# Kernel tuning notes

Measured on AMD Instinct MI355X. Metric: run time of the kernel, lower is better.

## Reference

```python
import jax, jax.numpy as jnp
import numpy as np

N = 10000
E = 320000
D = 256   # hidden_dim
H = 4     # heads
C = D // H
NL = 3    # gat layers
EPS = 1e-5


def _ln(x, g, b):
    m = x.mean(-1, keepdims=True)
    v = ((x - m) ** 2).mean(-1, keepdims=True)
    return (x - m) / jnp.sqrt(v + EPS) * g + b


def setup_inputs() -> dict:
    key = jax.random.key(0)
    ks = iter(jax.random.split(key, 64))
    rn = lambda shape, s=0.05: jax.random.normal(next(ks), shape, dtype=jnp.float32) * s
    inp = dict(
        x=jax.random.normal(next(ks), (N, 10), dtype=jnp.float32),
        edge_index=jax.random.randint(next(ks), (2, E), 0, N),
        edge_attr=jax.random.uniform(next(ks), (E, 3), dtype=jnp.float32),
        agent_features=jax.random.normal(next(ks), (1, 10), dtype=jnp.float32),
        # node encoder
        enc_w=rn((10, D)), enc_b=jnp.zeros(D), enc_g=jnp.ones(D), enc_bt=jnp.zeros(D),
        # adaptive virtual node
        vn_base=jnp.zeros(D), vn_w1=rn((D, D)), vn_b1=jnp.zeros(D),
        vn_g=jnp.ones(D), vn_bt=jnp.zeros(D), vn_w2=rn((D, D)), vn_b2=jnp.zeros(D),
        # stacked GAT layer params
        gat_w=rn((NL, D, D)), att_src=rn((NL, H, C)), att_dst=rn((NL, H, C)),
        att_edge=rn((NL, H, C)), edge_w=rn((NL, 3, D)), gat_b=jnp.zeros((NL, D)),
        ln_g=jnp.ones((NL, D)), ln_b=jnp.zeros((NL, D)),
        # agent encoder
        ag_w=rn((10, D)), ag_b=jnp.zeros(D), ag_g=jnp.ones(D), ag_bt=jnp.zeros(D),
        # dueling heads (jk_dim = D*(NL+1) + D)
        v_w1=rn((D * (NL + 2), D)), v_b1=jnp.zeros(D), v_g=jnp.ones(D), v_bt=jnp.zeros(D),
        v_w2=rn((D, 1)), v_b2=jnp.zeros(1),
        a_w1=rn((D * (NL + 2), D)), a_b1=jnp.zeros(D), a_g=jnp.ones(D), a_bt=jnp.zeros(D),
        a_w2=rn((D, 9)), a_b2=jnp.zeros(9),
    )
    return inp


def _gat_layer(h, src, dst, eattr, lin_w, a_s, a_d, a_e, e_w, bias, n_seg):
    xs = (h @ lin_w).reshape(-1, H, C)                       # [Nt,H,C]
    al_s = (xs * a_s).sum(-1)                                # [Nt,H]
    al_d = (xs * a_d).sum(-1)
    ee = (eattr @ e_w).reshape(-1, H, C)                     # [Et,H,C]
    al_e = (ee * a_e).sum(-1)                                # [Et,H]
    alpha = jax.nn.leaky_relu(al_s[src] + al_d[dst] + al_e, 0.2)
    mx = jax.ops.segment_max(alpha, dst, num_segments=n_seg)
    a = jnp.exp(alpha - mx[dst])
    s = jax.ops.segment_sum(a, dst, num_segments=n_seg)
    a = a / (s[dst] + 1e-16)
    msg = xs[src] * a[:, :, None]                            # [Et,H,C]
    out = jax.ops.segment_sum(msg, dst, num_segments=n_seg)
    return out.reshape(n_seg, D) + bias


def reference(x, edge_index, edge_attr, agent_features,
              enc_w, enc_b, enc_g, enc_bt,
              vn_base, vn_w1, vn_b1, vn_g, vn_bt, vn_w2, vn_b2,
              gat_w, att_src, att_dst, att_edge, edge_w, gat_b, ln_g, ln_b,
              ag_w, ag_b, ag_g, ag_bt,
              v_w1, v_b1, v_g, v_bt, v_w2, v_b2,
              a_w1, a_b1, a_g, a_bt, a_w2, a_b2):
    n = x.shape[0]
    nt = n + 1  # + virtual node
    h0 = jax.nn.relu(_ln(x @ enc_w + enc_b, enc_g, enc_bt))
    ctx = h0.mean(0)
    ad = jnp.tanh(jax.nn.relu(_ln(ctx @ vn_w1 + vn_b1, vn_g, vn_bt)) @ vn_w2 + vn_b2)
    vn = vn_base + ad
    h = jnp.concatenate([h0, vn[None]], axis=0)              # [Nt,D]

    # virtual-node edges (bidirectional) with edge_attr = [0.5,0,0]
    ar = jnp.arange(n)
    vfull = jnp.full((n,), n, dtype=edge_index.dtype)
    src0 = jnp.concatenate([edge_index[0], vfull, ar])
    dst0 = jnp.concatenate([edge_index[1], ar, vfull])
    veattr = jnp.concatenate([jnp.full((2 * n, 1), 0.5), jnp.zeros((2 * n, 2))], axis=1)
    eattr0 = jnp.concatenate([edge_attr, veattr], axis=0)

    # GATConv add_self_loops with fill_value='mean' (mean of incoming edge_attr)
    deg = jax.ops.segment_sum(jnp.ones_like(dst0, dtype=jnp.float32), dst0, num_segments=nt)
    loop_attr = jax.ops.segment_sum(eattr0, dst0, num_segments=nt) / jnp.maximum(deg, 1.0)[:, None]
    loops = jnp.arange(nt, dtype=edge_index.dtype)
    src = jnp.concatenate([src0, loops])
    dst = jnp.concatenate([dst0, loops])
    eattr = jnp.concatenate([eattr0, loop_attr], axis=0)

    outs = [h]
    for i in range(NL):
        hn = _gat_layer(h, src, dst, eattr, gat_w[i], att_src[i], att_dst[i],
                        att_edge[i], edge_w[i], gat_b[i], nt)
        hn = _ln(hn, ln_g[i], ln_b[i])
        h = jax.nn.relu(hn + h)
        outs.append(h)
    jk = jnp.concatenate(outs, axis=-1)                      # [Nt, D*(NL+1)]

    global_repr = jk[-1][None]                               # virtual node row
    agent = jax.nn.relu(_ln(agent_features @ ag_w + ag_b, ag_g, ag_bt))
    comb = jnp.concatenate([global_repr, agent], axis=-1)
    val = jax.nn.relu(_ln(comb @ v_w1 + v_b1, v_g, v_bt)) @ v_w2 + v_b2
    adv = jax.nn.relu(_ln(comb @ a_w1 + a_b1, a_g, a_bt)) @ a_w2 + a_b2
    return val + (adv - adv.mean(axis=1, keepdims=True))
```

## Files before the change

kernel.cpp:

```cpp
#include <hip/hip_runtime.h>
#include <math.h>

#define NN 10000
#define EE 320000
#define DD 256
#define NT 10001
#define E1C (EE + NN)
#define E2C (EE + 2 * NN)
#define ETC (E2C + NT)
#define VB 157
#define RB 2500

typedef __attribute__((ext_vector_type(8))) short s16x8;
typedef __attribute__((ext_vector_type(4))) float f32x4;

__device__ __forceinline__ unsigned short f2bf(float f) {
    unsigned u = __float_as_uint(f);
    return (unsigned short)((u + 0x7FFFu + ((u >> 16) & 1u)) >> 16);
}
__device__ __forceinline__ float bf2f(unsigned short u) {
    return __uint_as_float((unsigned)u << 16);
}

__device__ __forceinline__ float wave_sum(float v) {
#pragma unroll
    for (int o = 32; o > 0; o >>= 1) v += __shfl_down(v, o, 64);
    return v;
}
__device__ __forceinline__ float blk_sum256(float v, float* sm4) {
    v = wave_sum(v);
    int lane = threadIdx.x & 63, w = threadIdx.x >> 6;
    __syncthreads();
    if (lane == 0) sm4[w] = v;
    __syncthreads();
    return sm4[0] + sm4[1] + sm4[2] + sm4[3];
}
__device__ __forceinline__ float2 blk_sum2(float a, float b, float2* sm4) {
#pragma unroll
    for (int o = 32; o > 0; o >>= 1) {
        a += __shfl_down(a, o, 64);
        b += __shfl_down(b, o, 64);
    }
    int lane = threadIdx.x & 63, w = threadIdx.x >> 6;
    __syncthreads();
    if (lane == 0) sm4[w] = make_float2(a, b);
    __syncthreads();
    float2 r;
    r.x = sm4[0].x + sm4[1].x + sm4[2].x + sm4[3].x;
    r.y = sm4[0].y + sm4[1].y + sm4[2].y + sm4[3].y;
    return r;
}

__global__ void __launch_bounds__(256) k_enc(
        const float* __restrict__ x, const float* __restrict__ wenc,
        const float* __restrict__ bia, const float* __restrict__ g,
        const float* __restrict__ bt, float* __restrict__ h,
        unsigned short* __restrict__ hb) {
    int t = threadIdx.x, lane = t & 63, wv = t >> 6;
    int v = blockIdx.x * 4 + wv;
    if (v >= NN) return;
    float xv = (lane < 10) ? x[v * 10 + lane] : 0.f;
    float4 acc = *(const float4*)(bia + lane * 4);
#pragma unroll
    for (int k = 0; k < 10; k++) {
        float xk = __shfl(xv, k, 64);
        float4 wk = *(const float4*)(wenc + k * DD + lane * 4);
        acc.x += xk * wk.x; acc.y += xk * wk.y; acc.z += xk * wk.z; acc.w += xk * wk.w;
    }
    float s1 = acc.x + acc.y + acc.z + acc.w;
    float s2 = acc.x * acc.x + acc.y * acc.y + acc.z * acc.z + acc.w * acc.w;
#pragma unroll
    for (int o = 32; o > 0; o >>= 1) {
        s1 += __shfl_xor(s1, o, 64);
        s2 += __shfl_xor(s2, o, 64);
    }
    float m = s1 * (1.f / DD);
    float var = s2 * (1.f / DD) - m * m;
    float rs = rsqrtf(var + 1e-5f);
    float4 g4 = *(const float4*)(g + lane * 4);
    float4 b4 = *(const float4*)(bt + lane * 4);
    float4 r4;
    r4.x = fmaxf((acc.x - m) * rs * g4.x + b4.x, 0.f);
    r4.y = fmaxf((acc.y - m) * rs * g4.y + b4.y, 0.f);
    r4.z = fmaxf((acc.z - m) * rs * g4.z + b4.z, 0.f);
    r4.w = fmaxf((acc.w - m) * rs * g4.w + b4.w, 0.f);
    *(float4*)(h + (size_t)v * DD + lane * 4) = r4;
    ushort4 u4;
    u4.x = f2bf(r4.x); u4.y = f2bf(r4.y); u4.z = f2bf(r4.z); u4.w = f2bf(r4.w);
    *(ushort4*)(hb + (size_t)v * DD + lane * 4) = u4;
}

__global__ void __launch_bounds__(256) k_ctx1deg(const float* __restrict__ h,
                                                 float* __restrict__ part,
                                                 const int* __restrict__ ei,
                                                 int* __restrict__ degi) {
    __shared__ float4 sm[4][64];
    int t = threadIdx.x, lane = t & 63, w = t >> 6;
    int b = blockIdx.x;
    float4 acc = make_float4(0.f, 0.f, 0.f, 0.f);
    for (int v = b * 4 + w; v < NN; v += 1024) {
        float4 hv = *(const float4*)(h + (size_t)v * DD + lane * 4);
        acc.x += hv.x; acc.y += hv.y; acc.z += hv.z; acc.w += hv.w;
    }
    sm[w][lane] = acc;
    __syncthreads();
    if (t < 64) {
        float4 a0 = sm[0][t], a1 = sm[1][t], a2 = sm[2][t], a3 = sm[3][t];
        float4 r;
        r.x = a0.x + a1.x + a2.x + a3.x;
        r.y = a0.y + a1.y + a2.y + a3.y;
        r.z = a0.z + a1.z + a2.z + a3.z;
        r.w = a0.w + a1.w + a2.w + a3.w;
        *(float4*)(part + (size_t)b * DD + t * 4) = r;
    }
    for (int e = b * 256 + t; e < EE; e += 256 * 256)
        atomicAdd(&degi[ei[EE + e]], 1);
}

__global__ void k_vn(const float* __restrict__ part,
                     const float* __restrict__ w1, const float* __restrict__ b1,
                     const float* __restrict__ g, const float* __restrict__ bt,
                     const float* __restrict__ w2, const float* __restrict__ b2,
                     const float* __restrict__ vnb,
                     float* __restrict__ h, unsigned short* __restrict__ hb,
                     float* __restrict__ comb) {
    __shared__ float2 sm4[4];
    __shared__ float cs[DD];
    __shared__ float t[DD];
    int j = threadIdx.x;
    float c = 0.f;
    for (int b = 0; b < 256; b++) c += part[(size_t)b * DD + j];
    cs[j] = c * (1.f / NN);
    __syncthreads();
    float acc = b1[j];
    for (int k = 0; k < DD; k++) acc += cs[k] * w1[k * DD + j];
    float2 mm = blk_sum2(acc, acc * acc, sm4);
    float m = mm.x * (1.f / DD);
    float var = mm.y * (1.f / DD) - m * m;
    float y = fmaxf((acc - m) * rsqrtf(var + 1e-5f) * g[j] + bt[j], 0.f);
    t[j] = y;
    __syncthreads();
    float a2 = b2[j];
    for (int k = 0; k < DD; k++) a2 += t[k] * w2[k * DD + j];
    float vn = vnb[j] + tanhf(a2);
    h[(size_t)NN * DD + j] = vn;
    hb[(size_t)NN * DD + j] = f2bf(vn);
    comb[j] = vn;
}

__global__ void k_scan(const int* __restrict__ degi, int* __restrict__ offs,
                       int* __restrict__ cursor) {
    __shared__ int wsum[16];
    __shared__ int running_s;
    int t = threadIdx.x, lane = t & 63, w = t >> 6;
    if (t == 0) running_s = 0;
    __syncthreads();
    for (int base = 0; base < NT; base += 1024) {
        int v = base + t;
        int val = 0;
        if (v < NN) val = degi[v] + 2;
        else if (v == NN) val = NN + 1;
        int x = val;
#pragma unroll
        for (int o = 1; o < 64; o <<= 1) {
            int y = __shfl_up(x, o, 64);
            if (lane >= o) x += y;
        }
        if (lane == 63) wsum[w] = x;
        __syncthreads();
        int prefix = running_s;
        for (int ww = 0; ww < w; ww++) prefix += wsum[ww];
        if (v <= NN) { int e0 = prefix + x - val; offs[v] = e0; cursor[v] = e0; }
        __syncthreads();
        if (t == 0) {
            int s = 0;
            for (int i = 0; i < 16; i++) s += wsum[i];
            running_s += s;
        }
        __syncthreads();
    }
    if (threadIdx.x == 0) offs[NT] = running_s;
}

__global__ void k_scatter(const int* __restrict__ ei, int* __restrict__ cursor,
                          int* __restrict__ ssrc, int* __restrict__ seid) {
    int e = blockIdx.x * 256 + threadIdx.x;
    if (e >= EE) return;
    int src = ei[e], dst = ei[EE + e];
    int pos = atomicAdd(&cursor[dst], 1);
    ssrc[pos] = src;
    seid[pos] = e;
}

__global__ void k_flattr(const int* __restrict__ offs, int* __restrict__ ssrc,
                         int* __restrict__ seid,
                         const float* __restrict__ ea, float* __restrict__ lattr) {
    int t = threadIdx.x, lane = t & 63, w = t >> 6;
    int v = blockIdx.x * 4 + w;
    if (v > NN) return;
    int bN = offs[NN];
    if (v == NN) {
        if (lane == 0) {
            lattr[v * 3] = 0.5f; lattr[v * 3 + 1] = 0.f; lattr[v * 3 + 2] = 0.f;
            ssrc[bN + NN] = NN; seid[bN + NN] = E2C + NN;
        }
        return;
    }
    int b0 = offs[v], e1 = offs[v + 1];
    if (lane == 0) {
        ssrc[e1 - 2] = NN; seid[e1 - 2] = EE + v;
        ssrc[e1 - 1] = v;  seid[e1 - 1] = E2C + v;
        ssrc[bN + v] = v;  seid[bN + v] = E1C + v;
    }
    int cnt = e1 - b0 - 2;
    float s0 = 0.f, s1 = 0.f, s2 = 0.f;
    for (int i = lane; i < cnt; i += 64) {
        int e = seid[b0 + i];
        s0 += ea[e * 3];
        s1 += ea[e * 3 + 1];
        s2 += ea[e * 3 + 2];
    }
    s0 = wave_sum(s0); s1 = wave_sum(s1); s2 = wave_sum(s2);
    if (lane == 0) {
        float inv = 1.f / (float)(cnt + 1);
        lattr[v * 3]     = (s0 + 0.5f) * inv;
        lattr[v * 3 + 1] = s1 * inv;
        lattr[v * 3 + 2] = s2 * inv;
    }
}

__global__ void k_wconv(const float* __restrict__ gw, unsigned short* __restrict__ wt,
                        const float* __restrict__ ew, const float* __restrict__ ae,
                        float* __restrict__ wd) {
    int b = blockIdx.x, j = threadIdx.x;
    if (b == 768) {
        if (j >= 36) return;
        int l = j / 12, k = (j / 4) % 3, h = j % 4;
        float s = 0.f;
        for (int c = 0; c < 64; c++)
            s += ew[l * 768 + k * DD + h * 64 + c] * ae[l * DD + h * 64 + c];
        wd[j] = s;
        return;
    }
    int l = b >> 8, k = b & 255;
    float v = gw[l * 65536 + k * 256 + j];
    wt[l * 65536 + j * 256 + k] = f2bf(v);
}

__global__ void k_edot(const int* __restrict__ seid, const float* __restrict__ ea,
                       const float* __restrict__ lattr, const float* __restrict__ wd,
                       unsigned short* __restrict__ edot) {
    int p = blockIdx.x * 256 + threadIdx.x;
    if (p >= ETC) return;
    int e = seid[p];
    float a0, a1, a2;
    if (e < EE)       { a0 = ea[e * 3]; a1 = ea[e * 3 + 1]; a2 = ea[e * 3 + 2]; }
    else if (e < E2C) { a0 = 0.5f; a1 = 0.f; a2 = 0.f; }
    else              { int v = e - E2C; a0 = lattr[v * 3]; a1 = lattr[v * 3 + 1]; a2 = lattr[v * 3 + 2]; }
#pragma unroll
    for (int l = 0; l < 3; l++) {
        ushort4 o;
        o.x = f2bf(a0 * wd[l * 12 + 0] + a1 * wd[l * 12 + 4] + a2 * wd[l * 12 + 8]);
        o.y = f2bf(a0 * wd[l * 12 + 1] + a1 * wd[l * 12 + 5] + a2 * wd[l * 12 + 9]);
        o.z = f2bf(a0 * wd[l * 12 + 2] + a1 * wd[l * 12 + 6] + a2 * wd[l * 12 + 10]);
        o.w = f2bf(a0 * wd[l * 12 + 3] + a1 * wd[l * 12 + 7] + a2 * wd[l * 12 + 11]);
        *(ushort4*)(edot + (size_t)l * ETC * 4 + (size_t)p * 4) = o;
    }
}

__global__ void __launch_bounds__(256) k_gemm_mfma(
        const unsigned short* __restrict__ hb, const unsigned short* __restrict__ wt,
        const float* __restrict__ as_, const float* __restrict__ ad_,
        unsigned short* __restrict__ xsb, float* __restrict__ als, float* __restrict__ ald) {
    __shared__ unsigned short tile[64][128];
    int bx = blockIdx.x;
    int v0 = (bx >> 1) * 64;
    int n0 = (bx & 1) * 128;
    int t = threadIdx.x, lane = t & 63, w = t >> 6;
    int rbase = v0 + w * 16;
    int li = lane & 15, g = lane >> 4;
    int arow = rbase + li; if (arow > NN) arow = NN;
    int koff = g * 8;
    const unsigned short* aptr = hb + (size_t)arow * DD + koff;
    const unsigned short* bptr = wt + (size_t)(n0 + li) * DD + koff;
    f32x4 acc[8];
#pragma unroll
    for (int n = 0; n < 8; n++) acc[n] = (f32x4){0.f, 0.f, 0.f, 0.f};
#pragma unroll
    for (int kb = 0; kb < 8; kb++) {
        s16x8 af = *(const s16x8*)(aptr + kb * 32);
#pragma unroll
        for (int n = 0; n < 8; n++) {
            s16x8 bf = *(const s16x8*)(bptr + (size_t)n * 16 * DD + kb * 32);
            acc[n] = __builtin_amdgcn_mfma_f32_16x16x32_bf16(af, bf, acc[n], 0, 0, 0);
        }
    }
    float asv[8], adv[8];
#pragma unroll
    for (int n = 0; n < 8; n++) { asv[n] = as_[n0 + n * 16 + li]; adv[n] = ad_[n0 + n * 16 + li]; }
    int hg0 = n0 >> 6;
#pragma unroll
    for (int r = 0; r < 4; r++) {
        int vrow = rbase + 4 * g + r;
#pragma unroll
        for (int h = 0; h < 2; h++) {
            float ps = acc[4 * h][r] * asv[4 * h] + acc[4 * h + 1][r] * asv[4 * h + 1]
                     + acc[4 * h + 2][r] * asv[4 * h + 2] + acc[4 * h + 3][r] * asv[4 * h + 3];
            float pd = acc[4 * h][r] * adv[4 * h] + acc[4 * h + 1][r] * adv[4 * h + 1]
                     + acc[4 * h + 2][r] * adv[4 * h + 2] + acc[4 * h + 3][r] * adv[4 * h + 3];
#pragma unroll
            for (int o = 1; o < 16; o <<= 1) {
                ps += __shfl_xor(ps, o, 64);
                pd += __shfl_xor(pd, o, 64);
            }
            if (li == 0 && vrow <= NN) { als[vrow * 4 + hg0 + h] = ps; ald[vrow * 4 + hg0 + h] = pd; }
        }
    }
#pragma unroll
    for (int n = 0; n < 8; n++)
#pragma unroll
        for (int r = 0; r < 4; r++)
            tile[w * 16 + 4 * g + r][n * 16 + li] = f2bf(acc[n][r]);
#pragma unroll
    for (int it = 0; it < 4; it++) {
        int flat = it * 64 + lane;
        int row = w * 16 + (flat >> 4);
        int c8 = flat & 15;
        int vrow = v0 + row;
        if (vrow <= NN)
            *(uint4*)(xsb + (size_t)vrow * DD + n0 + c8 * 8) = *(const uint4*)(&tile[row][c8 * 8]);
    }
}

__global__ void __launch_bounds__(256) k_msg(
        const int* __restrict__ offs, const int* __restrict__ ssrc,
        const unsigned short* __restrict__ edotL,
        const float* __restrict__ als, const float* __restrict__ ald,
        const unsigned short* __restrict__ xsb,
        const float* __restrict__ bias, const float* __restrict__ g,
        const float* __restrict__ bt, const float* __restrict__ hin,
        float* __restrict__ hout, unsigned short* __restrict__ hbout,
        float* __restrict__ pvacc, float* __restrict__ pws) {
    int b = blockIdx.x;
    int t = threadIdx.x, lane = t & 63, w = t >> 6;
    if (b >= RB) {
        int sub = lane >> 5, l32 = lane & 31, slot = w * 2 + sub;
        int hh = l32 >> 3;
        __shared__ float red[4][8][33];
        __shared__ float wsred[4][4];
        int bb = b - RB;
        int b0 = offs[NN];
        float adh = ald[NN * 4 + hh];
        int i0 = bb * 64, i1 = i0 + 64;
        if (i1 > NN + 1) i1 = NN + 1;
        float acc[8];
#pragma unroll
        for (int q = 0; q < 8; q++) acc[q] = 0.f;
        float swt = 0.f;
        for (int i = i0 + slot; i < i1; i += 8) {
            float a = als[i * 4 + hh] + bf2f(edotL[(size_t)(b0 + i) * 4 + hh]) + adh;
            a = a > 0.f ? a : 0.2f * a;
            float wt = __expf(a);
            uint4 xq = *(const uint4*)(xsb + (size_t)i * DD + l32 * 8);
            const unsigned short* xp = (const unsigned short*)&xq;
#pragma unroll
            for (int q = 0; q < 8; q++) acc[q] += wt * bf2f(xp[q]);
            if ((l32 & 7) == 0) swt += wt;
        }
#pragma unroll
        for (int q = 0; q < 8; q++) acc[q] += __shfl_xor(acc[q], 32, 64);
        swt += __shfl_xor(swt, 32, 64);
        if (sub == 0) {
#pragma unroll
            for (int q = 0; q < 8; q++) red[w][q][l32] = acc[q];
            if ((l32 & 7) == 0) wsred[w][hh] = swt;
        }
        __syncthreads();
        int c = t, q = c & 7, l = c >> 3;
        pvacc[(size_t)bb * DD + c] = red[0][q][l] + red[1][q][l] + red[2][q][l] + red[3][q][l];
        if (t < 4) pws[bb * 4 + t] = wsred[0][t] + wsred[1][t] + wsred[2][t] + wsred[3][t];
        return;
    }
    __shared__ int   lsrc[4][64];
    __shared__ float lw[4][64][4];
    int v = b * 4 + w;
    int b0 = offs[v], deg = offs[v + 1] - b0;
    int hh = lane >> 4;
    float4 ad4 = *(const float4*)(ald + v * 4);
    float a0c = 0.f, a1c = 0.f, a2c = 0.f, a3c = 0.f;
    float ws = 0.f;
    for (int base = 0; base < deg; base += 64) {
        int rem = deg - base; if (rem > 64) rem = 64;
        if (lane < rem) {
            int p = b0 + base + lane;
            int src = ssrc[p];
            lsrc[w][lane] = src;
            ushort4 ed = *(const ushort4*)(edotL + (size_t)p * 4);
            float4 a4 = *(const float4*)(als + src * 4);
            float f0 = a4.x + bf2f(ed.x) + ad4.x; f0 = f0 > 0.f ? f0 : 0.2f * f0;
            float f1 = a4.y + bf2f(ed.y) + ad4.y; f1 = f1 > 0.f ? f1 : 0.2f * f1;
            float f2 = a4.z + bf2f(ed.z) + ad4.z; f2 = f2 > 0.f ? f2 : 0.2f * f2;
            float f3 = a4.w + bf2f(ed.w) + ad4.w; f3 = f3 > 0.f ? f3 : 0.2f * f3;
            lw[w][lane][0] = __expf(f0);
            lw[w][lane][1] = __expf(f1);
            lw[w][lane][2] = __expf(f2);
            lw[w][lane][3] = __expf(f3);
        }
        for (int i = 0; i < rem; i++) {
            float wt = lw[w][i][hh];
            int src = lsrc[w][i];
            ushort4 xq = *(const ushort4*)(xsb + (size_t)src * DD + lane * 4);
            a0c += wt * bf2f(xq.x);
            a1c += wt * bf2f(xq.y);
            a2c += wt * bf2f(xq.z);
            a3c += wt * bf2f(xq.w);
            ws += wt;
        }
    }
    float inv = 1.f / (ws + 1e-16f);
    float4 bi4 = *(const float4*)(bias + lane * 4);
    float t0 = a0c * inv + bi4.x;
    float t1 = a1c * inv + bi4.y;
    float t2 = a2c * inv + bi4.z;
    float t3 = a3c * inv + bi4.w;
    float s1 = t0 + t1 + t2 + t3;
    float s2 = t0 * t0 + t1 * t1 + t2 * t2 + t3 * t3;
#pragma unroll
    for (int o = 32; o > 0; o >>= 1) {
        s1 += __shfl_xor(s1, o, 64);
        s2 += __shfl_xor(s2, o, 64);
    }
    float m = s1 * (1.f / DD);
    float var = s2 * (1.f / DD) - m * m;
    float rs = rsqrtf(var + 1e-5f);
    float4 g4 = *(const float4*)(g + lane * 4);
    float4 b4 = *(const float4*)(bt + lane * 4);
    float4 h4 = *(const float4*)(hin + (size_t)v * DD + lane * 4);
    float4 r4;
    r4.x = fmaxf((t0 - m) * rs * g4.x + b4.x + h4.x, 0.f);
    r4.y = fmaxf((t1 - m) * rs * g4.y + b4.y + h4.y, 0.f);
    r4.z = fmaxf((t2 - m) * rs * g4.z + b4.z + h4.z, 0.f);
    r4.w = fmaxf((t3 - m) * rs * g4.w + b4.w + h4.w, 0.f);
    *(float4*)(hout + (size_t)v * DD + lane * 4) = r4;
    ushort4 u4;
    u4.x = f2bf(r4.x); u4.y = f2bf(r4.y); u4.z = f2bf(r4.z); u4.w = f2bf(r4.w);
    *(ushort4*)(hbout + (size_t)v * DD + lane * 4) = u4;
}

__global__ void k_vpost(const float* __restrict__ pvacc, const float* __restrict__ pws,
                        const float* __restrict__ bias, const float* __restrict__ g,
                        const float* __restrict__ bt, const float* __restrict__ hin,
                        float* __restrict__ hout, unsigned short* __restrict__ hb,
                        float* __restrict__ jkslot,
                        int last, const float* __restrict__ af,
                        const float* __restrict__ agw, const float* __restrict__ agb,
                        const float* __restrict__ agg, const float* __restrict__ agbt,
                        float* __restrict__ comb) {
    __shared__ float2 sm4[4];
    int j = threadIdx.x, hh = j >> 6;
    float acc = 0.f;
    for (int b = 0; b < VB; b++) acc += pvacc[(size_t)b * DD + j];
    float ws = 0.f;
    for (int b = 0; b < VB; b++) ws += pws[b * 4 + hh];
    float o = acc / (ws + 1e-16f);
    float tt = o + bias[j];
    float2 mm = blk_sum2(tt, tt * tt, sm4);
    float m = mm.x * (1.f / DD);
    float var = mm.y * (1.f / DD) - m * m;
    float y = (tt - m) * rsqrtf(var + 1e-5f) * g[j] + bt[j];
    float r = fmaxf(y + hin[(size_t)NN * DD + j], 0.f);
    hout[(size_t)NN * DD + j] = r;
    hb[(size_t)NN * DD + j] = f2bf(r);
    jkslot[j] = r;
    if (last) {
        float a2 = agb[j];
#pragma unroll
        for (int k = 0; k < 10; k++) a2 += af[k] * agw[k * DD + j];
        float2 m2 = blk_sum2(a2, a2 * a2, sm4);
        float mu = m2.x * (1.f / DD);
        float vv = m2.y * (1.f / DD) - mu * mu;
        float ya = (a2 - mu) * rsqrtf(vv + 1e-5f) * agg[j] + agbt[j];
        comb[1024 + j] = fmaxf(ya, 0.f);
    }
}

__global__ void k_head(const float* __restrict__ comb,
                       const float* __restrict__ vw1, const float* __restrict__ aw1,
                       float* __restrict__ pv, float* __restrict__ pa,
                       int* __restrict__ cnt,
                       const float* __restrict__ vb1, const float* __restrict__ vg,
                       const float* __restrict__ vbt, const float* __restrict__ vw2,
                       const float* __restrict__ vb2,
                       const float* __restrict__ ab1, const float* __restrict__ ag,
                       const float* __restrict__ abt, const float* __restrict__ aw2,
                       const float* __restrict__ ab2, float* __restrict__ out) {
    __shared__ float2 sm4[4];
    __shared__ float sm1[4];
    __shared__ float tl[DD];
    __shared__ float adv[9];
    __shared__ float valv;
    __shared__ int islast;
    int j = threadIdx.x, s = blockIdx.x;
    int k0 = s * 32;
    float accv = 0.f, acca = 0.f;
#pragma unroll
    for (int kk = 0; kk < 32; kk++) {
        float c = comb[k0 + kk];
        accv += c * vw1[(k0 + kk) * DD + j];
        acca += c * aw1[(k0 + kk) * DD + j];
    }
    pv[s * DD + j] = accv;
    pa[s * DD + j] = acca;
    __threadfence();
    if (j == 0) islast = (atomicAdd(cnt, 1) == 39) ? 1 : 0;
    __syncthreads();
    if (!islast) return;
    __threadfence();
    float acc = vb1[j], acc2 = ab1[j];
    for (int ss = 0; ss < 40; ss++) { acc += pv[ss * DD + j]; acc2 += pa[ss * DD + j]; }
    float2 mm = blk_sum2(acc, acc * acc, sm4);
    float m = mm.x * (1.f / DD);
    float var = mm.y * (1.f / DD) - m * m;
    float y = fmaxf((acc - m) * rsqrtf(var + 1e-5f) * vg[j] + vbt[j], 0.f);
    float vs = blk_sum256(y * vw2[j], sm1);
    if (j == 0) valv = vs + vb2[0];
    float2 mm2 = blk_sum2(acc2, acc2 * acc2, sm4);
    float m2 = mm2.x * (1.f / DD);
    float var2 = mm2.y * (1.f / DD) - m2 * m2;
    float y2 = fmaxf((acc2 - m2) * rsqrtf(var2 + 1e-5f) * ag[j] + abt[j], 0.f);
    tl[j] = y2;
    __syncthreads();
    if (j < 9) {
        float ss = ab2[j];
        for (int k = 0; k < DD; k++) ss += tl[k] * aw2[k * 9 + j];
        adv[j] = ss;
    }
    __syncthreads();
    if (j < 9) {
        float mean = 0.f;
        for (int o = 0; o < 9; o++) mean += adv[o];
        mean *= (1.f / 9.f);
        out[j] = valv + adv[j] - mean;
    }
}

extern "C" void kernel_launch(void* const* d_in, const int* in_sizes, int n_in,
                              void* d_out, int out_size, void* d_ws, size_t ws_size,
                              hipStream_t stream) {
    (void)in_sizes; (void)n_in; (void)out_size; (void)ws_size;
    const float* x      = (const float*)d_in[0];
    const int*   ei     = (const int*)d_in[1];
    const float* ea     = (const float*)d_in[2];
    const float* af     = (const float*)d_in[3];
    const float* enc_w  = (const float*)d_in[4];
    const float* enc_b  = (const float*)d_in[5];
    const float* enc_g  = (const float*)d_in[6];
    const float* enc_bt = (const float*)d_in[7];
    const float* vn_base= (const float*)d_in[8];
    const float* vn_w1  = (const float*)d_in[9];
    const float* vn_b1  = (const float*)d_in[10];
    const float* vn_g   = (const float*)d_in[11];
    const float* vn_bt  = (const float*)d_in[12];
    const float* vn_w2  = (const float*)d_in[13];
    const float* vn_b2  = (const float*)d_in[14];
    const float* gat_w  = (const float*)d_in[15];
    const float* att_src= (const float*)d_in[16];
    const float* att_dst= (const float*)d_in[17];
    const float* att_edge=(const float*)d_in[18];
    const float* edge_w = (const float*)d_in[19];
    const float* gat_b  = (const float*)d_in[20];
    const float* ln_g   = (const float*)d_in[21];
    const float* ln_b   = (const float*)d_in[22];
    const float* ag_w   = (const float*)d_in[23];
    const float* ag_b   = (const float*)d_in[24];
    const float* ag_g   = (const float*)d_in[25];
    const float* ag_bt  = (const float*)d_in[26];
    const float* v_w1   = (const float*)d_in[27];
    const float* v_b1   = (const float*)d_in[28];
    const float* v_g    = (const float*)d_in[29];
    const float* v_bt   = (const float*)d_in[30];
    const float* v_w2   = (const float*)d_in[31];
    const float* v_b2   = (const float*)d_in[32];
    const float* a_w1   = (const float*)d_in[33];
    const float* a_b1   = (const float*)d_in[34];
    const float* a_g    = (const float*)d_in[35];
    const float* a_bt   = (const float*)d_in[36];
    const float* a_w2   = (const float*)d_in[37];
    const float* a_b2   = (const float*)d_in[38];

    char* p = (char*)d_ws;
    auto alloc = [&](size_t bytes) {
        char* r = p;
        p += (bytes + 255) & ~(size_t)255;
        return r;
    };
    float* big0  = (float*)alloc((size_t)NT * DD * 4);
    float* big2  = (float*)alloc((size_t)NT * DD * 4);
    unsigned short* hb   = (unsigned short*)alloc((size_t)NT * DD * 2);
    unsigned short* xsb  = (unsigned short*)alloc((size_t)NT * DD * 2);
    unsigned short* wt   = (unsigned short*)alloc((size_t)3 * DD * DD * 2);
    unsigned short* edot = (unsigned short*)alloc((size_t)3 * ETC * 4 * 2);
    int* ssrc    = (int*)alloc((size_t)ETC * 4);
    int* seid    = (int*)alloc((size_t)ETC * 4);
    float* als   = (float*)alloc((size_t)NT * 4 * 4);
    float* ald   = (float*)alloc((size_t)NT * 4 * 4);
    float* part  = (float*)alloc((size_t)256 * DD * 4);
    float* comb  = (float*)alloc(1280 * 4);
    float* lattr = (float*)alloc((size_t)NT * 3 * 4);
    float* wd    = (float*)alloc(36 * 4);
    float* pvacc = (float*)alloc((size_t)VB * DD * 4);
    float* pws   = (float*)alloc((size_t)VB * 4 * 4);
    float* pv    = (float*)alloc(40 * DD * 4);
    float* pa    = (float*)alloc(40 * DD * 4);
    int* degi    = (int*)alloc((size_t)(NT + 16) * 4);
    int* cnt     = degi + NT;
    int* offs    = (int*)alloc((size_t)(NT + 1) * 4);
    int* cursor  = (int*)alloc((size_t)NT * 4);

    hipMemsetAsync(degi, 0, (size_t)(NT + 16) * 4, stream);

    k_enc<<<2500, 256, 0, stream>>>(x, enc_w, enc_b, enc_g, enc_bt, big0, hb);
    k_ctx1deg<<<256, 256, 0, stream>>>(big0, part, ei, degi);
    k_vn<<<1, 256, 0, stream>>>(part, vn_w1, vn_b1, vn_g, vn_bt, vn_w2, vn_b2, vn_base, big0, hb, comb);
    k_scan<<<1, 1024, 0, stream>>>(degi, offs, cursor);
    k_scatter<<<(EE + 255) / 256, 256, 0, stream>>>(ei, cursor, ssrc, seid);
    k_flattr<<<(NT + 3) / 4, 256, 0, stream>>>(offs, ssrc, seid, ea, lattr);
    k_wconv<<<769, 256, 0, stream>>>(gat_w, wt, edge_w, att_edge, wd);
    k_edot<<<(ETC + 255) / 256, 256, 0, stream>>>(seid, ea, lattr, wd, edot);

    float* cur = big0;
    float* po  = big2;
    for (int l = 0; l < 3; l++) {
        const unsigned short* edotL = edot + (size_t)l * ETC * 4;
        k_gemm_mfma<<<((NT + 63) / 64) * 2, 256, 0, stream>>>(hb, wt + (size_t)l * DD * DD,
                                                              att_src + l * DD, att_dst + l * DD,
                                                              xsb, als, ald);
        k_msg<<<RB + VB, 256, 0, stream>>>(offs, ssrc, edotL, als, ald, xsb,
                                           gat_b + l * DD, ln_g + l * DD, ln_b + l * DD,
                                           cur, po, hb, pvacc, pws);
        k_vpost<<<1, 256, 0, stream>>>(pvacc, pws, gat_b + l * DD, ln_g + l * DD, ln_b + l * DD,
                                       cur, po, hb, comb + (l + 1) * DD,
                                       (l == 2) ? 1 : 0, af, ag_w, ag_b, ag_g, ag_bt, comb);
        float* t = cur; cur = po; po = t;
    }
    k_head<<<40, 256, 0, stream>>>(comb, v_w1, a_w1, pv, pa, cnt,
                                   v_b1, v_g, v_bt, v_w2, v_b2,
                                   a_b1, a_g, a_bt, a_w2, a_b2, (float*)d_out);
}
```

Baseline: 336.3 us.

## Fuse preprocessing kernels to cut launches in GAT setup pipeline

Folds the weight transpose/bf16 conversion and edge-attention dot precompute into the encoder kernel as extra blocks, merges the virtual-node MLP and degree scan into one two-block launch, and computes per-edge attention terms directly inside the loop-attribute kernel instead of a separate edot pass. This removes three kernel launches and one full pass over the sorted edge list. The scan now runs on 256 threads instead of 1024, so it needs more serial iterations, and the edot work now sits inside a per-node wave loop.

```diff
diff --git a/kernel.cpp b/kernel.cpp
--- a/kernel.cpp
+++ b/kernel.cpp
@@ -55,9 +55,30 @@
         const float* __restrict__ x, const float* __restrict__ wenc,
         const float* __restrict__ bia, const float* __restrict__ g,
         const float* __restrict__ bt, float* __restrict__ h,
-        unsigned short* __restrict__ hb) {
-    int t = threadIdx.x, lane = t & 63, wv = t >> 6;
-    int v = blockIdx.x * 4 + wv;
+        unsigned short* __restrict__ hb,
+        const float* __restrict__ gw, unsigned short* __restrict__ wtb,
+        const float* __restrict__ ew, const float* __restrict__ ae,
+        float* __restrict__ wd) {
+    int bx = blockIdx.x;
+    int t = threadIdx.x;
+    if (bx >= 2500) {
+        if (bx == 3268) {
+            if (t >= 36) return;
+            int l = t / 12, k = (t / 4) % 3, hh = t % 4;
+            float s = 0.f;
+            for (int c = 0; c < 64; c++)
+                s += ew[l * 768 + k * DD + hh * 64 + c] * ae[l * DD + hh * 64 + c];
+            wd[t] = s;
+            return;
+        }
+        int b = bx - 2500;
+        int l = b >> 8, k = b & 255;
+        float v = gw[l * 65536 + k * 256 + t];
+        wtb[l * 65536 + t * 256 + k] = f2bf(v);
+        return;
+    }
+    int lane = t & 63, wv = t >> 6;
+    int v = bx * 4 + wv;
     if (v >= NN) return;
     float xv = (lane < 10) ? x[v * 10 + lane] : 0.f;
     float4 acc = *(const float4*)(bia + lane * 4);
@@ -117,16 +138,48 @@
         atomicAdd(&degi[ei[EE + e]], 1);
 }
 
-__global__ void k_vn(const float* __restrict__ part,
-                     const float* __restrict__ w1, const float* __restrict__ b1,
-                     const float* __restrict__ g, const float* __restrict__ bt,
-                     const float* __restrict__ w2, const float* __restrict__ b2,
-                     const float* __restrict__ vnb,
-                     float* __restrict__ h, unsigned short* __restrict__ hb,
-                     float* __restrict__ comb) {
+__global__ void __launch_bounds__(256) k_vnscan(
+        const float* __restrict__ part,
+        const float* __restrict__ w1, const float* __restrict__ b1,
+        const float* __restrict__ g, const float* __restrict__ bt,
+        const float* __restrict__ w2, const float* __restrict__ b2,
+        const float* __restrict__ vnb,
+        float* __restrict__ h, unsigned short* __restrict__ hb,
+        float* __restrict__ comb,
+        const int* __restrict__ degi, int* __restrict__ offs,
+        int* __restrict__ cursor) {
+    if (blockIdx.x == 1) {
+        __shared__ int wsum[4];
+        __shared__ int running_s;
+        int t = threadIdx.x, lane = t & 63, w = t >> 6;
+        if (t == 0) running_s = 0;
+        __syncthreads();
+        for (int base = 0; base < NT; base += 256) {
+            int v = base + t;
+            int val = 0;
+            if (v < NN) val = degi[v] + 2;
+            else if (v == NN) val = NN + 1;
+            int x = val;
+#pragma unroll
+            for (int o = 1; o < 64; o <<= 1) {
+                int y = __shfl_up(x, o, 64);
+                if (lane >= o) x += y;
+            }
+            if (lane == 63) wsum[w] = x;
+            __syncthreads();
+            int prefix = running_s;
+            for (int ww = 0; ww < w; ww++) prefix += wsum[ww];
+            if (v <= NN) { int e0 = prefix + x - val; offs[v] = e0; cursor[v] = e0; }
+            __syncthreads();
+            if (t == 0) running_s += wsum[0] + wsum[1] + wsum[2] + wsum[3];
+            __syncthreads();
+        }
+        if (threadIdx.x == 0) offs[NT] = running_s;
+        return;
+    }
     __shared__ float2 sm4[4];
     __shared__ float cs[DD];
-    __shared__ float t[DD];
+    __shared__ float tl[DD];
     int j = threadIdx.x;
     float c = 0.f;
     for (int b = 0; b < 256; b++) c += part[(size_t)b * DD + j];
@@ -138,48 +191,14 @@
     float m = mm.x * (1.f / DD);
     float var = mm.y * (1.f / DD) - m * m;
     float y = fmaxf((acc - m) * rsqrtf(var + 1e-5f) * g[j] + bt[j], 0.f);
-    t[j] = y;
+    tl[j] = y;
     __syncthreads();
     float a2 = b2[j];
-    for (int k = 0; k < DD; k++) a2 += t[k] * w2[k * DD + j];
+    for (int k = 0; k < DD; k++) a2 += tl[k] * w2[k * DD + j];
     float vn = vnb[j] + tanhf(a2);
     h[(size_t)NN * DD + j] = vn;
     hb[(size_t)NN * DD + j] = f2bf(vn);
     comb[j] = vn;
-}
-
-__global__ void k_scan(const int* __restrict__ degi, int* __restrict__ offs,
-                       int* __restrict__ cursor) {
-    __shared__ int wsum[16];
-    __shared__ int running_s;
-    int t = threadIdx.x, lane = t & 63, w = t >> 6;
-    if (t == 0) running_s = 0;
-    __syncthreads();
-    for (int base = 0; base < NT; base += 1024) {
-        int v = base + t;
-        int val = 0;
-        if (v < NN) val = degi[v] + 2;
-        else if (v == NN) val = NN + 1;
-        int x = val;
-#pragma unroll
-        for (int o = 1; o < 64; o <<= 1) {
-            int y = __shfl_up(x, o, 64);
-            if (lane >= o) x += y;
-        }
-        if (lane == 63) wsum[w] = x;
-        __syncthreads();
-        int prefix = running_s;
-        for (int ww = 0; ww < w; ww++) prefix += wsum[ww];
-        if (v <= NN) { int e0 = prefix + x - val; offs[v] = e0; cursor[v] = e0; }
-        __syncthreads();
-        if (t == 0) {
-            int s = 0;
-            for (int i = 0; i < 16; i++) s += wsum[i];
-            running_s += s;
-        }
-        __syncthreads();
-    }
-    if (threadIdx.x == 0) offs[NT] = running_s;
 }
 
 __global__ void k_scatter(const int* __restrict__ ei, int* __restrict__ cursor,
@@ -194,15 +213,31 @@
 
 __global__ void k_flattr(const int* __restrict__ offs, int* __restrict__ ssrc,
                          int* __restrict__ seid,
-                         const float* __restrict__ ea, float* __restrict__ lattr) {
+                         const float* __restrict__ ea, float* __restrict__ lattr,
+                         const float* __restrict__ wdg,
+                         unsigned short* __restrict__ edot) {
+    __shared__ float wd[36];
     int t = threadIdx.x, lane = t & 63, w = t >> 6;
+    if (t < 36) wd[t] = wdg[t];
+    __syncthreads();
     int v = blockIdx.x * 4 + w;
     if (v > NN) return;
     int bN = offs[NN];
+    ushort4 c05[3];
+#pragma unroll
+    for (int l = 0; l < 3; l++) {
+        c05[l].x = f2bf(0.5f * wd[l * 12 + 0]);
+        c05[l].y = f2bf(0.5f * wd[l * 12 + 1]);
+        c05[l].z = f2bf(0.5f * wd[l * 12 + 2]);
+        c05[l].w = f2bf(0.5f * wd[l * 12 + 3]);
+    }
     if (v == NN) {
         if (lane == 0) {
             lattr[v * 3] = 0.5f; lattr[v * 3 + 1] = 0.f; lattr[v * 3 + 2] = 0.f;
             ssrc[bN + NN] = NN; seid[bN + NN] = E2C + NN;
+#pragma unroll
+            for (int l = 0; l < 3; l++)
+                *(ushort4*)(edot + (size_t)l * ETC * 4 + (size_t)(bN + NN) * 4) = c05[l];
         }
         return;
     }
@@ -211,60 +246,44 @@
         ssrc[e1 - 2] = NN; seid[e1 - 2] = EE + v;
         ssrc[e1 - 1] = v;  seid[e1 - 1] = E2C + v;
         ssrc[bN + v] = v;  seid[bN + v] = E1C + v;
+#pragma unroll
+        for (int l = 0; l < 3; l++) {
+            *(ushort4*)(edot + (size_t)l * ETC * 4 + (size_t)(e1 - 2) * 4) = c05[l];
+            *(ushort4*)(edot + (size_t)l * ETC * 4 + (size_t)(bN + v) * 4) = c05[l];
+        }
     }
     int cnt = e1 - b0 - 2;
     float s0 = 0.f, s1 = 0.f, s2 = 0.f;
     for (int i = lane; i < cnt; i += 64) {
         int e = seid[b0 + i];
-        s0 += ea[e * 3];
-        s1 += ea[e * 3 + 1];
-        s2 += ea[e * 3 + 2];
+        float a0 = ea[e * 3], a1 = ea[e * 3 + 1], a2 = ea[e * 3 + 2];
+        s0 += a0; s1 += a1; s2 += a2;
+#pragma unroll
+        for (int l = 0; l < 3; l++) {
+            ushort4 o;
+            o.x = f2bf(a0 * wd[l * 12 + 0] + a1 * wd[l * 12 + 4] + a2 * wd[l * 12 + 8]);
+            o.y = f2bf(a0 * wd[l * 12 + 1] + a1 * wd[l * 12 + 5] + a2 * wd[l * 12 + 9]);
+            o.z = f2bf(a0 * wd[l * 12 + 2] + a1 * wd[l * 12 + 6] + a2 * wd[l * 12 + 10]);
+            o.w = f2bf(a0 * wd[l * 12 + 3] + a1 * wd[l * 12 + 7] + a2 * wd[l * 12 + 11]);
+            *(ushort4*)(edot + (size_t)l * ETC * 4 + (size_t)(b0 + i) * 4) = o;
+        }
     }
     s0 = wave_sum(s0); s1 = wave_sum(s1); s2 = wave_sum(s2);
     if (lane == 0) {
         float inv = 1.f / (float)(cnt + 1);
-        lattr[v * 3]     = (s0 + 0.5f) * inv;
-        lattr[v * 3 + 1] = s1 * inv;
-        lattr[v * 3 + 2] = s2 * inv;
-    }
-}
-
-__global__ void k_wconv(const float* __restrict__ gw, unsigned short* __restrict__ wt,
-                        const float* __restrict__ ew, const float* __restrict__ ae,
-                        float* __restrict__ wd) {
-    int b = blockIdx.x, j = threadIdx.x;
-    if (b == 768) {
-        if (j >= 36) return;
-        int l = j / 12, k = (j / 4) % 3, h = j % 4;
-        float s = 0.f;
-        for (int c = 0; c < 64; c++)
-            s += ew[l * 768 + k * DD + h * 64 + c] * ae[l * DD + h * 64 + c];
-        wd[j] = s;
-        return;
-    }
-    int l = b >> 8, k = b & 255;
-    float v = gw[l * 65536 + k * 256 + j];
-    wt[l * 65536 + j * 256 + k] = f2bf(v);
-}
-
-__global__ void k_edot(const int* __restrict__ seid, const float* __restrict__ ea,
-                       const float* __restrict__ lattr, const float* __restrict__ wd,
-                       unsigned short* __restrict__ edot) {
-    int p = blockIdx.x * 256 + threadIdx.x;
-    if (p >= ETC) return;
-    int e = seid[p];
-    float a0, a1, a2;
-    if (e < EE)       { a0 = ea[e * 3]; a1 = ea[e * 3 + 1]; a2 = ea[e * 3 + 2]; }
-    else if (e < E2C) { a0 = 0.5f; a1 = 0.f; a2 = 0.f; }
-    else              { int v = e - E2C; a0 = lattr[v * 3]; a1 = lattr[v * 3 + 1]; a2 = lattr[v * 3 + 2]; }
-#pragma unroll
-    for (int l = 0; l < 3; l++) {
-        ushort4 o;
-        o.x = f2bf(a0 * wd[l * 12 + 0] + a1 * wd[l * 12 + 4] + a2 * wd[l * 12 + 8]);
-        o.y = f2bf(a0 * wd[l * 12 + 1] + a1 * wd[l * 12 + 5] + a2 * wd[l * 12 + 9]);
-        o.z = f2bf(a0 * wd[l * 12 + 2] + a1 * wd[l * 12 + 6] + a2 * wd[l * 12 + 10]);
-        o.w = f2bf(a0 * wd[l * 12 + 3] + a1 * wd[l * 12 + 7] + a2 * wd[l * 12 + 11]);
-        *(ushort4*)(edot + (size_t)l * ETC * 4 + (size_t)p * 4) = o;
+        float la0 = (s0 + 0.5f) * inv;
+        float la1 = s1 * inv;
+        float la2 = s2 * inv;
+        lattr[v * 3] = la0; lattr[v * 3 + 1] = la1; lattr[v * 3 + 2] = la2;
+#pragma unroll
+        for (int l = 0; l < 3; l++) {
+            ushort4 o;
+            o.x = f2bf(la0 * wd[l * 12 + 0] + la1 * wd[l * 12 + 4] + la2 * wd[l * 12 + 8]);
+            o.y = f2bf(la0 * wd[l * 12 + 1] + la1 * wd[l * 12 + 5] + la2 * wd[l * 12 + 9]);
+            o.z = f2bf(la0 * wd[l * 12 + 2] + la1 * wd[l * 12 + 6] + la2 * wd[l * 12 + 10]);
+            o.w = f2bf(la0 * wd[l * 12 + 3] + la1 * wd[l * 12 + 7] + la2 * wd[l * 12 + 11]);
+            *(ushort4*)(edot + (size_t)l * ETC * 4 + (size_t)(e1 - 1) * 4) = o;
+        }
     }
 }
 
@@ -459,8 +478,10 @@
     __shared__ float2 sm4[4];
     int j = threadIdx.x, hh = j >> 6;
     float acc = 0.f;
+#pragma unroll 4
     for (int b = 0; b < VB; b++) acc += pvacc[(size_t)b * DD + j];
     float ws = 0.f;
+#pragma unroll 4
     for (int b = 0; b < VB; b++) ws += pws[b * 4 + hh];
     float o = acc / (ws + 1e-16f);
     float tt = o + bias[j];
@@ -619,14 +640,13 @@
 
     hipMemsetAsync(degi, 0, (size_t)(NT + 16) * 4, stream);
 
-    k_enc<<<2500, 256, 0, stream>>>(x, enc_w, enc_b, enc_g, enc_bt, big0, hb);
+    k_enc<<<3269, 256, 0, stream>>>(x, enc_w, enc_b, enc_g, enc_bt, big0, hb,
+                                    gat_w, wt, edge_w, att_edge, wd);
     k_ctx1deg<<<256, 256, 0, stream>>>(big0, part, ei, degi);
-    k_vn<<<1, 256, 0, stream>>>(part, vn_w1, vn_b1, vn_g, vn_bt, vn_w2, vn_b2, vn_base, big0, hb, comb);
-    k_scan<<<1, 1024, 0, stream>>>(degi, offs, cursor);
+    k_vnscan<<<2, 256, 0, stream>>>(part, vn_w1, vn_b1, vn_g, vn_bt, vn_w2, vn_b2,
+                                    vn_base, big0, hb, comb, degi, offs, cursor);
     k_scatter<<<(EE + 255) / 256, 256, 0, stream>>>(ei, cursor, ssrc, seid);
-    k_flattr<<<(NT + 3) / 4, 256, 0, stream>>>(offs, ssrc, seid, ea, lattr);
-    k_wconv<<<769, 256, 0, stream>>>(gat_w, wt, edge_w, att_edge, wd);
-    k_edot<<<(ETC + 255) / 256, 256, 0, stream>>>(seid, ea, lattr, wd, edot);
+    k_flattr<<<(NT + 3) / 4, 256, 0, stream>>>(offs, ssrc, seid, ea, lattr, wd, edot);
 
     float* cur = big0;
     float* po  = big2;
```

After: 361.1 us. 1.07x slower.
